# Optimization experiments

Hardware: AMD Instinct MI355X
Metric: run time of the kernel (lower is better)

Reference implementation:

```python
import jax, jax.numpy as jnp
import numpy as np

EPS = 1e-05
IFAVERAGE = True


def setup_inputs() -> dict:
    key = jax.random.key(0)
    k1, k2 = jax.random.split(key)
    B, C = 4, 5
    D = H = W = 128
    inp = jax.random.normal(k1, (B, C, D, H, W), dtype=jnp.float32)
    tgt = jax.random.randint(k2, (B, D, H, W), 0, C, dtype=jnp.int64)
    return {"input": inp, "target": tgt}


def reference(input, target):
    B, C = input.shape[0], input.shape[1]
    x = input.reshape(B, C, -1)          # (B, C, N)
    t = target.reshape(B, -1)            # (B, N)
    pred = jnp.argmax(x, axis=1)         # (B, N) int, matches torch.max(dim=-2) indices

    def per_batch_counts(p, tg):
        pred_c = jnp.bincount(p, length=C)                              # (C,)
        tgt_c = jnp.bincount(tg, length=C)                              # (C,)
        # intersection: count positions where pred == target, binned by class
        inter_c = jnp.bincount(jnp.where(p == tg, p, C), length=C + 1)[:C]
        return pred_c, tgt_c, inter_c

    pred_c, tgt_c, inter_c = jax.vmap(per_batch_counts)(pred, t)        # each (B, C)

    # classes 1..C-1 (background class 0 excluded)
    inter = inter_c[:, 1:].astype(jnp.float32)
    union = (pred_c[:, 1:] + tgt_c[:, 1:]).astype(jnp.float32)
    dice = (2.0 * inter + EPS) / (union + EPS)                          # (B, C-1)

    if IFAVERAGE:
        out = jnp.mean(jnp.mean(dice, axis=0), axis=0, keepdims=True)   # shape (1,)
    else:
        out = dice
    return out
```

## Files before the change

kernel.cpp:

```cpp
#include <hip/hip_runtime.h>


static constexpr int   kB   = 4;
static constexpr int   kC   = 5;
static constexpr int   kN   = 128 * 128 * 128;
static constexpr float kEPS = 1e-5f;

static constexpr int TPB = 256;
static constexpr int VPT = 2;
static constexpr int GPB = TPB * VPT;
static constexpr int BLOCKS_PER_BATCH = (kN / 4) / GPB;
static constexpr int kNumCnt = kB * 12;

__device__ __forceinline__ int argmax5(float v0, float v1, float v2, float v3, float v4) {
    int bi = 0; float bv = v0;
    if (v1 > bv) { bv = v1; bi = 1; }
    if (v2 > bv) { bv = v2; bi = 2; }
    if (v3 > bv) { bv = v3; bi = 3; }
    if (v4 > bv) { bv = v4; bi = 4; }
    return bi;
}

__device__ __forceinline__ void acc1(int p, int t,
                                     unsigned& P, unsigned& T, unsigned& I) {
    unsigned pm = p ? (1u << ((p - 1) << 3)) : 0u;
    unsigned tm = t ? (1u << ((t - 1) << 3)) : 0u;
    P += pm;
    T += tm;
    I += (p == t) ? pm : 0u;
}

__global__ __launch_bounds__(TPB) void dice_count_kernel(
        const float* __restrict__ in, const int* __restrict__ tgt,
        unsigned* __restrict__ cnt)
{
    const int b   = blockIdx.x >> 10;
    const int blk = blockIdx.x & 1023;
    const float* inb = in  + (size_t)b * kC * kN;
    const int*   tb  = tgt + (size_t)b * kN;

    const float4* c0 = (const float4*)(inb + 0 * (size_t)kN);
    const float4* c1 = (const float4*)(inb + 1 * (size_t)kN);
    const float4* c2 = (const float4*)(inb + 2 * (size_t)kN);
    const float4* c3 = (const float4*)(inb + 3 * (size_t)kN);
    const float4* c4 = (const float4*)(inb + 4 * (size_t)kN);
    const int4*   tp = (const int4*)tb;

    const int base = blk * GPB + threadIdx.x;

    float4 v[VPT][5];
    int4   tv[VPT];
#pragma unroll
    for (int i = 0; i < VPT; ++i) {
        const int n4 = base + i * TPB;
        v[i][0] = c0[n4];
        v[i][1] = c1[n4];
        v[i][2] = c2[n4];
        v[i][3] = c3[n4];
        v[i][4] = c4[n4];
        tv[i]   = tp[n4];
    }

    unsigned P = 0, T = 0, I = 0;
#pragma unroll
    for (int i = 0; i < VPT; ++i) {
        acc1(argmax5(v[i][0].x, v[i][1].x, v[i][2].x, v[i][3].x, v[i][4].x), tv[i].x, P, T, I);
        acc1(argmax5(v[i][0].y, v[i][1].y, v[i][2].y, v[i][3].y, v[i][4].y), tv[i].y, P, T, I);
        acc1(argmax5(v[i][0].z, v[i][1].z, v[i][2].z, v[i][3].z, v[i][4].z), tv[i].z, P, T, I);
        acc1(argmax5(v[i][0].w, v[i][1].w, v[i][2].w, v[i][3].w, v[i][4].w), tv[i].w, P, T, I);
    }

    unsigned r[6];
    r[0] = P & 0x00FF00FFu;  r[1] = (P >> 8) & 0x00FF00FFu;
    r[2] = T & 0x00FF00FFu;  r[3] = (T >> 8) & 0x00FF00FFu;
    r[4] = I & 0x00FF00FFu;  r[5] = (I >> 8) & 0x00FF00FFu;

#pragma unroll
    for (int k = 0; k < 6; ++k) {
#pragma unroll
        for (int off = 32; off > 0; off >>= 1) {
            r[k] += (unsigned)__shfl_down((int)r[k], off, 64);
        }
    }

    __shared__ unsigned sred[4][6];
    const int wave = threadIdx.x >> 6;
    if ((threadIdx.x & 63) == 0) {
#pragma unroll
        for (int k = 0; k < 6; ++k) sred[wave][k] = r[k];
    }
    __syncthreads();

    if (threadIdx.x < 6) {
        const int j = threadIdx.x;
        unsigned s = sred[0][j] + sred[1][j] + sred[2][j] + sred[3][j];
        const int g   = j >> 1;
        const int kLo = j & 1;
        unsigned* dst = cnt + b * 12 + g * 4;
        atomicAdd(&dst[kLo],     s & 0xFFFFu);
        atomicAdd(&dst[kLo + 2], s >> 16);
    }
}

__global__ void dice_final_kernel(const unsigned* __restrict__ cnt,
                                  float* __restrict__ out)
{
    if (threadIdx.x == 0 && blockIdx.x == 0) {
        float s = 0.0f;
#pragma unroll
        for (int b = 0; b < kB; ++b) {
#pragma unroll
            for (int k = 0; k < 4; ++k) {
                float pr = (float)cnt[b * 12 + 0 * 4 + k];
                float tg = (float)cnt[b * 12 + 1 * 4 + k];
                float it = (float)cnt[b * 12 + 2 * 4 + k];
                s += (2.0f * it + kEPS) / (pr + tg + kEPS);
            }
        }
        out[0] = s * (1.0f / 16.0f);
    }
}

extern "C" void kernel_launch(void* const* d_in, const int* in_sizes, int n_in,
                              void* d_out, int out_size, void* d_ws, size_t ws_size,
                              hipStream_t stream) {
    const float* in  = (const float*)d_in[0];
    const int*   tgt = (const int*)d_in[1];
    float*       out = (float*)d_out;
    unsigned*    cnt = (unsigned*)d_ws;

    hipMemsetAsync(cnt, 0, kNumCnt * sizeof(unsigned), stream);

    dice_count_kernel<<<dim3(kB * BLOCKS_PER_BATCH), dim3(TPB), 0, stream>>>(in, tgt, cnt);
    dice_final_kernel<<<1, 64, 0, stream>>>(cnt, out);
}
```

Measured before the change: 280.5 us.

## Replace atomics and memset with per-block partials and a single reduce kernel

The count kernel now writes each block's 12 packed counts to a per-block partial buffer instead of issuing global atomics. This removes the memset launch and atomic contention. Each thread also processes 4 iterations in a loop instead of 2 fully unrolled ones, which halves the block count to 2048. A new 256-thread reduce kernel sums the partials and computes the dice average in parallel. The risk is lower memory-level parallelism per thread and an extra pass over the partials.

```diff
diff --git a/kernel.cpp b/kernel.cpp
--- a/kernel.cpp
+++ b/kernel.cpp
@@ -6,11 +6,11 @@
 static constexpr int   kN   = 128 * 128 * 128;
 static constexpr float kEPS = 1e-5f;
 
-static constexpr int TPB = 256;
-static constexpr int VPT = 2;
-static constexpr int GPB = TPB * VPT;
-static constexpr int BLOCKS_PER_BATCH = (kN / 4) / GPB;
-static constexpr int kNumCnt = kB * 12;
+static constexpr int TPB   = 256;
+static constexpr int ITERS = 4;
+static constexpr int GPB   = TPB * ITERS;
+static constexpr int BPB   = (kN / 4) / GPB;
+static constexpr int NBLK  = kB * BPB;
 
 __device__ __forceinline__ int argmax5(float v0, float v1, float v2, float v3, float v4) {
     int bi = 0; float bv = v0;
@@ -32,10 +32,11 @@
 
 __global__ __launch_bounds__(TPB) void dice_count_kernel(
         const float* __restrict__ in, const int* __restrict__ tgt,
-        unsigned* __restrict__ cnt)
+        unsigned* __restrict__ partial)
 {
-    const int b   = blockIdx.x >> 10;
-    const int blk = blockIdx.x & 1023;
+    const int bg  = blockIdx.x;
+    const int b   = bg >> 9;
+    const int blk = bg & 511;
     const float* inb = in  + (size_t)b * kC * kN;
     const int*   tb  = tgt + (size_t)b * kN;
 
@@ -48,26 +49,20 @@
 
     const int base = blk * GPB + threadIdx.x;
 
-    float4 v[VPT][5];
-    int4   tv[VPT];
-#pragma unroll
-    for (int i = 0; i < VPT; ++i) {
+    unsigned P = 0, T = 0, I = 0;
+#pragma unroll 2
+    for (int i = 0; i < ITERS; ++i) {
         const int n4 = base + i * TPB;
-        v[i][0] = c0[n4];
-        v[i][1] = c1[n4];
-        v[i][2] = c2[n4];
-        v[i][3] = c3[n4];
-        v[i][4] = c4[n4];
-        tv[i]   = tp[n4];
-    }
-
-    unsigned P = 0, T = 0, I = 0;
-#pragma unroll
-    for (int i = 0; i < VPT; ++i) {
-        acc1(argmax5(v[i][0].x, v[i][1].x, v[i][2].x, v[i][3].x, v[i][4].x), tv[i].x, P, T, I);
-        acc1(argmax5(v[i][0].y, v[i][1].y, v[i][2].y, v[i][3].y, v[i][4].y), tv[i].y, P, T, I);
-        acc1(argmax5(v[i][0].z, v[i][1].z, v[i][2].z, v[i][3].z, v[i][4].z), tv[i].z, P, T, I);
-        acc1(argmax5(v[i][0].w, v[i][1].w, v[i][2].w, v[i][3].w, v[i][4].w), tv[i].w, P, T, I);
+        float4 v0 = c0[n4];
+        float4 v1 = c1[n4];
+        float4 v2 = c2[n4];
+        float4 v3 = c3[n4];
+        float4 v4 = c4[n4];
+        int4   t4 = tp[n4];
+        acc1(argmax5(v0.x, v1.x, v2.x, v3.x, v4.x), t4.x, P, T, I);
+        acc1(argmax5(v0.y, v1.y, v2.y, v3.y, v4.y), t4.y, P, T, I);
+        acc1(argmax5(v0.z, v1.z, v2.z, v3.z, v4.z), t4.z, P, T, I);
+        acc1(argmax5(v0.w, v1.w, v2.w, v3.w, v4.w), t4.w, P, T, I);
     }
 
     unsigned r[6];
@@ -96,28 +91,67 @@
         unsigned s = sred[0][j] + sred[1][j] + sred[2][j] + sred[3][j];
         const int g   = j >> 1;
         const int kLo = j & 1;
-        unsigned* dst = cnt + b * 12 + g * 4;
-        atomicAdd(&dst[kLo],     s & 0xFFFFu);
-        atomicAdd(&dst[kLo + 2], s >> 16);
+        unsigned* dst = partial + bg * 12 + g * 4;
+        dst[kLo]     = s & 0xFFFFu;
+        dst[kLo + 2] = s >> 16;
     }
 }
 
-__global__ void dice_final_kernel(const unsigned* __restrict__ cnt,
-                                  float* __restrict__ out)
+__global__ __launch_bounds__(256) void dice_reduce_kernel(
+        const unsigned* __restrict__ partial, float* __restrict__ out)
 {
-    if (threadIdx.x == 0 && blockIdx.x == 0) {
-        float s = 0.0f;
+    unsigned acc[4][12];
 #pragma unroll
-        for (int b = 0; b < kB; ++b) {
+    for (int b = 0; b < 4; ++b)
 #pragma unroll
-            for (int k = 0; k < 4; ++k) {
-                float pr = (float)cnt[b * 12 + 0 * 4 + k];
-                float tg = (float)cnt[b * 12 + 1 * 4 + k];
-                float it = (float)cnt[b * 12 + 2 * 4 + k];
-                s += (2.0f * it + kEPS) / (pr + tg + kEPS);
-            }
-        }
-        out[0] = s * (1.0f / 16.0f);
+        for (int j = 0; j < 12; ++j) acc[b][j] = 0;
+
+#pragma unroll
+    for (int c = 0; c < 8; ++c) {
+        const int b  = c >> 1;
+        const int bg = c * 256 + threadIdx.x;
+        const uint4* p = (const uint4*)(partial + bg * 12);
+        uint4 x = p[0], y = p[1], z = p[2];
+        acc[b][0] += x.x; acc[b][1]  += x.y; acc[b][2]  += x.z; acc[b][3]  += x.w;
+        acc[b][4] += y.x; acc[b][5]  += y.y; acc[b][6]  += y.z; acc[b][7]  += y.w;
+        acc[b][8] += z.x; acc[b][9]  += z.y; acc[b][10] += z.z; acc[b][11] += z.w;
+    }
+
+#pragma unroll
+    for (int b = 0; b < 4; ++b)
+#pragma unroll
+        for (int j = 0; j < 12; ++j)
+#pragma unroll
+            for (int off = 32; off > 0; off >>= 1)
+                acc[b][j] += (unsigned)__shfl_down((int)acc[b][j], off, 64);
+
+    __shared__ unsigned part[4][48];
+    const int wave = threadIdx.x >> 6;
+    if ((threadIdx.x & 63) == 0) {
+#pragma unroll
+        for (int b = 0; b < 4; ++b)
+#pragma unroll
+            for (int j = 0; j < 12; ++j) part[wave][b * 12 + j] = acc[b][j];
+    }
+    __syncthreads();
+
+    __shared__ unsigned tot[48];
+    if (threadIdx.x < 48) {
+        const int t = threadIdx.x;
+        tot[t] = part[0][t] + part[1][t] + part[2][t] + part[3][t];
+    }
+    __syncthreads();
+
+    if (threadIdx.x < 16) {
+        const int b = threadIdx.x >> 2;
+        const int k = threadIdx.x & 3;
+        float pr = (float)tot[b * 12 + 0 + k];
+        float tg = (float)tot[b * 12 + 4 + k];
+        float it = (float)tot[b * 12 + 8 + k];
+        float d = (2.0f * it + kEPS) / (pr + tg + kEPS);
+#pragma unroll
+        for (int off = 8; off > 0; off >>= 1) d += __shfl_down(d, off, 16);
+        if (threadIdx.x == 0) out[0] = d * (1.0f / 16.0f);
     }
 }
 
@@ -127,10 +161,8 @@
     const float* in  = (const float*)d_in[0];
     const int*   tgt = (const int*)d_in[1];
     float*       out = (float*)d_out;
-    unsigned*    cnt = (unsigned*)d_ws;
+    unsigned*    partial = (unsigned*)d_ws;
 
-    hipMemsetAsync(cnt, 0, kNumCnt * sizeof(unsigned), stream);
-
-    dice_count_kernel<<<dim3(kB * BLOCKS_PER_BATCH), dim3(TPB), 0, stream>>>(in, tgt, cnt);
-    dice_final_kernel<<<1, 64, 0, stream>>>(cnt, out);
+    dice_count_kernel<<<dim3(NBLK), dim3(TPB), 0, stream>>>(in, tgt, partial);
+    dice_reduce_kernel<<<dim3(1), dim3(256), 0, stream>>>(partial, out);
 }
```

Measured after the change: 254.9 us. 1.1x faster.
